# Optimization experiments

Hardware: AMD Instinct MI355X
Metric: run time of the kernel (lower is better)

## Reference

```python
import jax, jax.numpy as jnp
import numpy as np

N_NODES = 100000
N_EDGES = 1000000
D = 64
N_LAYERS = 3
LN_EPS = 1e-5


def setup_inputs() -> dict:
    key = jax.random.key(0)
    ks = jax.random.split(key, 12)
    s = 1.0 / np.sqrt(D)
    return {
        "feats": jax.random.normal(ks[0], (N_NODES, D), jnp.float32),
        "src": jax.random.randint(ks[1], (N_EDGES,), 0, N_NODES, jnp.int32),
        "dst": jax.random.randint(ks[2], (N_EDGES,), 0, N_NODES, jnp.int32),
        # GraphConv weights/biases (stacked over layers; in==hid==out==D)
        "conv_W": jax.random.normal(ks[3], (N_LAYERS, D, D), jnp.float32) * s,
        "conv_b": jnp.zeros((N_LAYERS, D), jnp.float32),
        # residual Linear per layer
        "res_W": jax.random.normal(ks[4], (N_LAYERS, D, D), jnp.float32) * s,
        "res_b": jnp.zeros((N_LAYERS, D), jnp.float32),
        # LayerNorm affine per layer
        "ln_g": jnp.ones((N_LAYERS, D), jnp.float32),
        "ln_b": jnp.zeros((N_LAYERS, D), jnp.float32),
        # final linear_prediction
        "pred_W": jax.random.normal(ks[5], (D, D), jnp.float32) * s,
        "pred_b": jnp.zeros((D,), jnp.float32),
    }


def _layer_norm(h, g, b):
    mu = jnp.mean(h, axis=-1, keepdims=True)
    var = jnp.mean(jnp.square(h - mu), axis=-1, keepdims=True)
    return (h - mu) * jax.lax.rsqrt(var + LN_EPS) * g + b


def reference(feats, src, dst, conv_W, conv_b, res_W, res_b, ln_g, ln_b, pred_W, pred_b):
    n = feats.shape[0]
    ones = jnp.ones(src.shape[0], feats.dtype)
    # DGL GraphConv norm='both', degrees clamped to >= 1
    out_deg = jnp.clip(jax.ops.segment_sum(ones, src, num_segments=n), 1.0, None)
    in_deg = jnp.clip(jax.ops.segment_sum(ones, dst, num_segments=n), 1.0, None)
    out_norm = jax.lax.rsqrt(out_deg)[:, None]  # [N,1]
    in_norm = jax.lax.rsqrt(in_deg)[:, None]

    h = feats
    h_final = jnp.zeros_like(feats)
    for i in range(N_LAYERS):
        # GraphConv: scale src, sum-aggregate over edges, scale dst, linear
        msg = (h * out_norm)[src]                                   # [E, D]
        agg = jax.ops.segment_sum(msg, dst, num_segments=n) * in_norm
        conv = agg @ conv_W[i] + conv_b[i]
        # residual linear + LayerNorm + relu (dropout p=0) + JK accumulate
        h = conv + h @ res_W[i] + res_b[i]
        h = jax.nn.relu(_layer_norm(h, ln_g[i], ln_b[i]))
        h_final = h_final + h
    return h_final @ pred_W + pred_b
```

## Files before the change

kernel.cpp:

```cpp
#include <hip/hip_runtime.h>
#include <hip/hip_bf16.h>

#define DD 64
#define NBLK 128
#define MAXBUK 1024
#define BSHIFT 7

typedef __attribute__((ext_vector_type(8))) short short8v;
typedef __attribute__((ext_vector_type(4))) float f32x4;

__device__ __forceinline__ unsigned pk_bf16(float a, float b) {
    __hip_bfloat162 h = __float22bfloat162_rn(make_float2(a, b));
    unsigned u; __builtin_memcpy(&u, &h, 4); return u;
}
__device__ __forceinline__ short f2bf_s(float f) {
    union { float f; unsigned u; } x; x.f = f;
    unsigned r = x.u + 0x7fff + ((x.u >> 16) & 1);
    return (short)(r >> 16);
}
__device__ __forceinline__ float bf_lo(unsigned u) { return __int_as_float(u << 16); }
__device__ __forceinline__ float bf_hi(unsigned u) { return __int_as_float(u & 0xffff0000u); }
__device__ __forceinline__ short8v u4_to_s8(uint4 u) {
    union { uint4 u; short8v s; } x; x.u = u; return x.s;
}
__device__ __forceinline__ int ofs_at(const int* __restrict__ c,
                                      const int* __restrict__ bs, int i) {
    return c[i] + bs[i >> 8];
}


__global__ __launch_bounds__(256) void part_count(
        const int* __restrict__ src, const int* __restrict__ dst,
        int* __restrict__ cnt, int E, int nbuk, int ce) {
    __shared__ int hd[MAXBUK], hs[MAXBUK];
    for (int i = threadIdx.x; i < MAXBUK; i += 256) { hd[i] = 0; hs[i] = 0; }
    __syncthreads();
    int e0 = blockIdx.x * ce;
    int e1 = min(e0 + ce, E);
    for (int e = e0 + (int)threadIdx.x; e < e1; e += 256) {
        atomicAdd(&hd[dst[e] >> BSHIFT], 1);
        atomicAdd(&hs[src[e] >> BSHIFT], 1);
    }
    __syncthreads();
    int L2 = nbuk * NBLK;
    for (int b = threadIdx.x; b < nbuk; b += 256) {
        cnt[b * NBLK + blockIdx.x]      = hd[b];
        cnt[L2 + b * NBLK + blockIdx.x] = hs[b];
    }
}

__global__ void scan1p(int* __restrict__ a, int* __restrict__ bsums, int L) {
    __shared__ int tmp[256];
    int gid = blockIdx.x * 256 + threadIdx.x;
    int v = (gid < L) ? a[gid] : 0;
    tmp[threadIdx.x] = v;
    __syncthreads();
    for (int off = 1; off < 256; off <<= 1) {
        int t = (threadIdx.x >= off) ? tmp[threadIdx.x - off] : 0;
        __syncthreads();
        tmp[threadIdx.x] += t;
        __syncthreads();
    }
    if (gid < L) a[gid] = tmp[threadIdx.x] - v;
    if (threadIdx.x == 255) bsums[blockIdx.x] = tmp[255];
}
__global__ void scan2p(int* __restrict__ bsums, int nb) {
    __shared__ int tmp[1024];
    int v = (threadIdx.x < (unsigned)nb) ? bsums[threadIdx.x] : 0;
    tmp[threadIdx.x] = v;
    __syncthreads();
    for (int off = 1; off < 1024; off <<= 1) {
        int t = (threadIdx.x >= off) ? tmp[threadIdx.x - off] : 0;
        __syncthreads();
        tmp[threadIdx.x] += t;
        __syncthreads();
    }
    if (threadIdx.x < (unsigned)nb) bsums[threadIdx.x] = tmp[threadIdx.x] - v;
}

__global__ __launch_bounds__(256) void part_scatter(
        const int* __restrict__ src, const int* __restrict__ dst,
        const int* __restrict__ cnt, const int* __restrict__ bsA,
        unsigned int* __restrict__ partD, unsigned char* __restrict__ partS,
        int E, int nbuk, int ce) {
    __shared__ int cd[MAXBUK], cs[MAXBUK];
    int L2 = nbuk * NBLK;
    for (int b = threadIdx.x; b < nbuk; b += 256) {
        cd[b] = ofs_at(cnt, bsA, b * NBLK + blockIdx.x);
        cs[b] = ofs_at(cnt, bsA, L2 + b * NBLK + blockIdx.x) - E;
    }
    __syncthreads();
    int e0 = blockIdx.x * ce;
    int e1 = min(e0 + ce, E);
    for (int e = e0 + (int)threadIdx.x; e < e1; e += 256) {
        int s = src[e], d = dst[e];
        int pd = atomicAdd(&cd[d >> BSHIFT], 1);
        partD[pd] = ((unsigned)(d & 127) << 17) | (unsigned)s;
        int ps = atomicAdd(&cs[s >> BSHIFT], 1);
        partS[ps] = (unsigned char)(s & 127);
    }
}

__global__ __launch_bounds__(256) void bucket_all(
        const unsigned int* __restrict__ partD, const unsigned char* __restrict__ partS,
        const int* __restrict__ cnt, const int* __restrict__ bsA,
        int* __restrict__ rowptr, int* __restrict__ esrc,
        float* __restrict__ inn, float* __restrict__ outn, float* __restrict__ rs,
        int E, int nbuk, int n) {
    __shared__ int hi[128], sc[128], cu[128], ho[128];
    int b = blockIdx.x, tid = threadIdx.x;
    int L2 = nbuk * NBLK;
    int e0 = ofs_at(cnt, bsA, b * NBLK);
    int e1 = (b + 1 < nbuk) ? ofs_at(cnt, bsA, (b + 1) * NBLK) : E;
    int f0 = ofs_at(cnt, bsA, L2 + b * NBLK) - E;
    int f1 = (b + 1 < nbuk) ? ofs_at(cnt, bsA, L2 + (b + 1) * NBLK) - E : E;
    if (tid < 128) { hi[tid] = 0; ho[tid] = 0; }
    __syncthreads();
    for (int e = e0 + tid; e < e1; e += 256) atomicAdd(&hi[partD[e] >> 17], 1);
    for (int e = f0 + tid; e < f1; e += 256) atomicAdd(&ho[(int)partS[e]], 1);
    __syncthreads();
    if (tid < 128) sc[tid] = hi[tid];
    __syncthreads();
    for (int off = 1; off < 128; off <<= 1) {
        int t = (tid < 128 && tid >= off) ? sc[tid - off] : 0;
        __syncthreads();
        if (tid < 128) sc[tid] += t;
        __syncthreads();
    }
    if (tid < 128) {
        int excl = e0 + sc[tid] - hi[tid];
        cu[tid] = excl;
        int v = (b << BSHIFT) + tid;
        if (v < n) {
            rowptr[v] = excl;
            inn[v] = rsqrtf((float)max(hi[tid], 1));
            float oc = (float)max(ho[tid], 1);
            outn[v] = rsqrtf(oc);
            rs[v]   = sqrtf(oc);
        }
    }
    if (b == 0 && tid == 0) rowptr[n] = E;
    __syncthreads();
    for (int e = e0 + tid; e < e1; e += 256) {
        unsigned u = partD[e];
        int p = atomicAdd(&cu[u >> 17], 1);
        esrc[p] = (int)(u & 0x1FFFFu);
    }
}

__global__ void scale_kernel(const float* __restrict__ feats, const float* __restrict__ outn,
                             unsigned short* __restrict__ hs, int n) {
    int idx = blockIdx.x * blockDim.x + threadIdx.x;
    if (idx < n * 8) {
        int v = idx >> 3;
        float s = outn[v];
        const float4* fp = (const float4*)feats + (size_t)idx * 2;
        float4 f0 = fp[0], f1 = fp[1];
        uint4 o;
        o.x = pk_bf16(f0.x * s, f0.y * s); o.y = pk_bf16(f0.z * s, f0.w * s);
        o.z = pk_bf16(f1.x * s, f1.y * s); o.w = pk_bf16(f1.z * s, f1.w * s);
        ((uint4*)hs)[idx] = o;
    }
}

__global__ __launch_bounds__(256) void gcn_kernel(
    const int* __restrict__ rowptr, const int* __restrict__ esrc,
    const float* __restrict__ inn, const float* __restrict__ rs,
    const float* __restrict__ outn,
    const unsigned short* __restrict__ hs_in,
    const float* __restrict__ Wc, const float* __restrict__ bc,
    const float* __restrict__ Wr, const float* __restrict__ br,
    const float* __restrict__ Wp, const float* __restrict__ pb,
    const float* __restrict__ g, const float* __restrict__ bb,
    unsigned short* __restrict__ hs_out, float* __restrict__ h_final,
    float* __restrict__ pred_out,
    int first, int last, int n)
{
    __shared__ __align__(16) short sWf[24 * 64 * 8];
    __shared__ __align__(16) short sXa[4][16 * 72];
    __shared__ float sEps[4 * 64];

    int lane = threadIdx.x & 63;
    int wave = threadIdx.x >> 6;
    int q   = lane & 15;
    int gg  = lane >> 4;
    int q8  = lane & 7;
    int o8  = lane >> 3;

    for (int idx = threadIdx.x; idx < 64; idx += blockDim.x) {
        sEps[idx]       = bc[idx] + br[idx];
        sEps[64 + idx]  = g[idx];
        sEps[128 + idx] = bb[idx];
        sEps[192 + idx] = pb[idx];
    }
    for (int f = wave * 6; f < wave * 6 + 6; ++f) {
        int mat = f >> 3, ft = (f >> 1) & 3, kc = f & 1;
        const float* Ws = (mat == 0) ? Wc : (mat == 1) ? Wr : Wp;
        int feat = ft * 16 + q;
        int k0 = kc * 32 + gg * 8;
        short8v fr;
        #pragma unroll
        for (int j = 0; j < 8; ++j) fr[j] = f2bf_s(Ws[(k0 + j) * DD + feat]);
        *(short8v*)&sWf[(f * 64 + lane) * 8] = fr;
    }
    __syncthreads();

    short* xrow_w = &sXa[wave][0];
    const short8v* wf = (const short8v*)sWf;
    int wgid = blockIdx.x * 4 + wave;
    int nwav = gridDim.x * 4;
    int ngrp = (n + 15) >> 4;

    for (int grp = wgid; grp < ngrp; grp += nwav) {
        int vbase = grp << 4;
        int vo = vbase + q;
        int vsel = min(vo, n - 1);

        const uint4* hrow = (const uint4*)(hs_in + (size_t)vsel * DD);
        uint4 bh0u = hrow[gg];
        uint4 bh1u = hrow[4 + gg];
        float rsv  = rs[vsel];
        float innv = inn[vsel];

        int rp = rowptr[min(vbase + min(lane, 16), n)];
        int stA = __shfl(rp, o8);     int dgA = __shfl(rp, o8 + 1) - stA;
        int stB = __shfl(rp, o8 + 8); int dgB = __shfl(rp, o8 + 9) - stB;

        #pragma unroll
        for (int hh = 0; hh < 2; ++hh) {
            int st = hh ? stB : stA;
            int dg = hh ? dgB : dgA;
            int mdg = dg;
            mdg = max(mdg, __shfl_xor(mdg, 8));
            mdg = max(mdg, __shfl_xor(mdg, 16));
            mdg = max(mdg, __shfl_xor(mdg, 32));

            float a[8];
            #pragma unroll
            for (int c = 0; c < 8; ++c) a[c] = 0.0f;

            int id0 = (0 < dg) ? esrc[st + 0] : 0;  float m0 = (0 < dg) ? 1.f : 0.f;
            int id1 = (1 < dg) ? esrc[st + 1] : 0;  float m1 = (1 < dg) ? 1.f : 0.f;
            int id2 = (2 < dg) ? esrc[st + 2] : 0;  float m2 = (2 < dg) ? 1.f : 0.f;
            int id3 = (3 < dg) ? esrc[st + 3] : 0;  float m3 = (3 < dg) ? 1.f : 0.f;

            for (int t = 0; t < mdg; t += 4) {
                uint4 r0 = *(const uint4*)(hs_in + (size_t)id0 * DD + q8 * 8);
                uint4 r1 = *(const uint4*)(hs_in + (size_t)id1 * DD + q8 * 8);
                uint4 r2 = *(const uint4*)(hs_in + (size_t)id2 * DD + q8 * 8);
                uint4 r3 = *(const uint4*)(hs_in + (size_t)id3 * DD + q8 * 8);
                float c0 = m0, c1 = m1, c2 = m2, c3 = m3;
                int t4 = t + 4;
                id0 = (t4 + 0 < dg) ? esrc[st + t4 + 0] : 0;  m0 = (t4 + 0 < dg) ? 1.f : 0.f;
                id1 = (t4 + 1 < dg) ? esrc[st + t4 + 1] : 0;  m1 = (t4 + 1 < dg) ? 1.f : 0.f;
                id2 = (t4 + 2 < dg) ? esrc[st + t4 + 2] : 0;  m2 = (t4 + 2 < dg) ? 1.f : 0.f;
                id3 = (t4 + 3 < dg) ? esrc[st + t4 + 3] : 0;  m3 = (t4 + 3 < dg) ? 1.f : 0.f;
                a[0] = fmaf(bf_lo(r0.x), c0, a[0]); a[1] = fmaf(bf_hi(r0.x), c0, a[1]);
                a[2] = fmaf(bf_lo(r0.y), c0, a[2]); a[3] = fmaf(bf_hi(r0.y), c0, a[3]);
                a[4] = fmaf(bf_lo(r0.z), c0, a[4]); a[5] = fmaf(bf_hi(r0.z), c0, a[5]);
                a[6] = fmaf(bf_lo(r0.w), c0, a[6]); a[7] = fmaf(bf_hi(r0.w), c0, a[7]);
                a[0] = fmaf(bf_lo(r1.x), c1, a[0]); a[1] = fmaf(bf_hi(r1.x), c1, a[1]);
                a[2] = fmaf(bf_lo(r1.y), c1, a[2]); a[3] = fmaf(bf_hi(r1.y), c1, a[3]);
                a[4] = fmaf(bf_lo(r1.z), c1, a[4]); a[5] = fmaf(bf_hi(r1.z), c1, a[5]);
                a[6] = fmaf(bf_lo(r1.w), c1, a[6]); a[7] = fmaf(bf_hi(r1.w), c1, a[7]);
                a[0] = fmaf(bf_lo(r2.x), c2, a[0]); a[1] = fmaf(bf_hi(r2.x), c2, a[1]);
                a[2] = fmaf(bf_lo(r2.y), c2, a[2]); a[3] = fmaf(bf_hi(r2.y), c2, a[3]);
                a[4] = fmaf(bf_lo(r2.z), c2, a[4]); a[5] = fmaf(bf_hi(r2.z), c2, a[5]);
                a[6] = fmaf(bf_lo(r2.w), c2, a[6]); a[7] = fmaf(bf_hi(r2.w), c2, a[7]);
                a[0] = fmaf(bf_lo(r3.x), c3, a[0]); a[1] = fmaf(bf_hi(r3.x), c3, a[1]);
                a[2] = fmaf(bf_lo(r3.y), c3, a[2]); a[3] = fmaf(bf_hi(r3.y), c3, a[3]);
                a[4] = fmaf(bf_lo(r3.z), c3, a[4]); a[5] = fmaf(bf_hi(r3.z), c3, a[5]);
                a[6] = fmaf(bf_lo(r3.w), c3, a[6]); a[7] = fmaf(bf_hi(r3.w), c3, a[7]);
            }

            uint4 w4;
            w4.x = pk_bf16(a[0], a[1]); w4.y = pk_bf16(a[2], a[3]);
            w4.z = pk_bf16(a[4], a[5]); w4.w = pk_bf16(a[6], a[7]);
            *(uint4*)&xrow_w[(hh * 8 + o8) * 72 + q8 * 8] = w4;
        }

        const short* xr = &xrow_w[q * 72];
        short8v ba0 = *(const short8v*)&xr[gg * 8];
        short8v ba1 = *(const short8v*)&xr[32 + gg * 8];
        short8v sh0 = u4_to_s8(bh0u);
        short8v sh1 = u4_to_s8(bh1u);

        f32x4 accC[4], accR[4];
        #pragma unroll
        for (int ft = 0; ft < 4; ++ft) {
            f32x4 c = {0.f, 0.f, 0.f, 0.f};
            c = __builtin_amdgcn_mfma_f32_16x16x32_bf16(wf[(ft * 2 + 0) * 64 + lane], ba0, c, 0, 0, 0);
            c = __builtin_amdgcn_mfma_f32_16x16x32_bf16(wf[(ft * 2 + 1) * 64 + lane], ba1, c, 0, 0, 0);
            accC[ft] = c;
            f32x4 r = {0.f, 0.f, 0.f, 0.f};
            r = __builtin_amdgcn_mfma_f32_16x16x32_bf16(wf[(8 + ft * 2 + 0) * 64 + lane], sh0, r, 0, 0, 0);
            r = __builtin_amdgcn_mfma_f32_16x16x32_bf16(wf[(8 + ft * 2 + 1) * 64 + lane], sh1, r, 0, 0, 0);
            accR[ft] = r;
        }

        f32x4 ac[4];
        #pragma unroll
        for (int ft = 0; ft < 4; ++ft) {
            float4 b4 = *(const float4*)&sEps[ft * 16 + gg * 4];
            ac[ft][0] = fmaf(innv, accC[ft][0], fmaf(rsv, accR[ft][0], b4.x));
            ac[ft][1] = fmaf(innv, accC[ft][1], fmaf(rsv, accR[ft][1], b4.y));
            ac[ft][2] = fmaf(innv, accC[ft][2], fmaf(rsv, accR[ft][2], b4.z));
            ac[ft][3] = fmaf(innv, accC[ft][3], fmaf(rsv, accR[ft][3], b4.w));
        }
        float s = 0.f;
        #pragma unroll
        for (int ft = 0; ft < 4; ++ft) s += ac[ft][0] + ac[ft][1] + ac[ft][2] + ac[ft][3];
        s += __shfl_xor(s, 16); s += __shfl_xor(s, 32);
        float mu = s * (1.0f / 64.0f);
        float vsum = 0.f;
        #pragma unroll
        for (int ft = 0; ft < 4; ++ft) {
            #pragma unroll
            for (int r = 0; r < 4; ++r) { float d = ac[ft][r] - mu; vsum += d * d; }
        }
        vsum += __shfl_xor(vsum, 16); vsum += __shfl_xor(vsum, 32);
        float rinv = rsqrtf(vsum * (1.0f / 64.0f) + 1e-5f);

        float4 yv[4];
        #pragma unroll
        for (int ft = 0; ft < 4; ++ft) {
            float4 g4 = *(const float4*)&sEps[64 + ft * 16 + gg * 4];
            float4 c4 = *(const float4*)&sEps[128 + ft * 16 + gg * 4];
            yv[ft].x = fmaxf((ac[ft][0] - mu) * rinv * g4.x + c4.x, 0.f);
            yv[ft].y = fmaxf((ac[ft][1] - mu) * rinv * g4.y + c4.y, 0.f);
            yv[ft].z = fmaxf((ac[ft][2] - mu) * rinv * g4.z + c4.z, 0.f);
            yv[ft].w = fmaxf((ac[ft][3] - mu) * rinv * g4.w + c4.w, 0.f);
        }

        if (!last) {
            if (vo < n) {
                float on = outn[vo];
                #pragma unroll
                for (int ft = 0; ft < 4; ++ft) {
                    size_t off = (size_t)vo * DD + ft * 16 + gg * 4;
                    uint2 p;
                    p.x = pk_bf16(yv[ft].x * on, yv[ft].y * on);
                    p.y = pk_bf16(yv[ft].z * on, yv[ft].w * on);
                    *(uint2*)&hs_out[off] = p;
                    if (first) {
                        *(float4*)&h_final[off] = yv[ft];
                    } else {
                        float4 hf = *(const float4*)&h_final[off];
                        hf.x += yv[ft].x; hf.y += yv[ft].y;
                        hf.z += yv[ft].z; hf.w += yv[ft].w;
                        *(float4*)&h_final[off] = hf;
                    }
                }
            }
        } else {
            #pragma unroll
            for (int ft = 0; ft < 4; ++ft) {
                float4 hf = make_float4(0.f, 0.f, 0.f, 0.f);
                if (vo < n) {
                    float4 old = *(const float4*)&h_final[(size_t)vo * DD + ft * 16 + gg * 4];
                    hf.x = old.x + yv[ft].x; hf.y = old.y + yv[ft].y;
                    hf.z = old.z + yv[ft].z; hf.w = old.w + yv[ft].w;
                }
                uint2 p;
                p.x = pk_bf16(hf.x, hf.y);
                p.y = pk_bf16(hf.z, hf.w);
                *(uint2*)&xrow_w[q * 72 + ft * 16 + gg * 4] = p;
            }
            short8v bp0 = *(const short8v*)&xr[gg * 8];
            short8v bp1 = *(const short8v*)&xr[32 + gg * 8];
            #pragma unroll
            for (int ft = 0; ft < 4; ++ft) {
                f32x4 p = {0.f, 0.f, 0.f, 0.f};
                p = __builtin_amdgcn_mfma_f32_16x16x32_bf16(wf[(16 + ft * 2 + 0) * 64 + lane], bp0, p, 0, 0, 0);
                p = __builtin_amdgcn_mfma_f32_16x16x32_bf16(wf[(16 + ft * 2 + 1) * 64 + lane], bp1, p, 0, 0, 0);
                if (vo < n) {
                    float4 b4 = *(const float4*)&sEps[192 + ft * 16 + gg * 4];
                    float4 o = make_float4(p[0] + b4.x, p[1] + b4.y, p[2] + b4.z, p[3] + b4.w);
                    *(float4*)&pred_out[(size_t)vo * DD + ft * 16 + gg * 4] = o;
                }
            }
        }
    }
}

extern "C" void kernel_launch(void* const* d_in, const int* in_sizes, int n_in,
                              void* d_out, int out_size, void* d_ws, size_t ws_size,
                              hipStream_t stream) {
    const float* feats  = (const float*)d_in[0];
    const int*   src    = (const int*)d_in[1];
    const int*   dst    = (const int*)d_in[2];
    const float* conv_W = (const float*)d_in[3];
    const float* conv_b = (const float*)d_in[4];
    const float* res_W  = (const float*)d_in[5];
    const float* res_b  = (const float*)d_in[6];
    const float* ln_g   = (const float*)d_in[7];
    const float* ln_b   = (const float*)d_in[8];
    const float* pred_W = (const float*)d_in[9];
    const float* pred_b = (const float*)d_in[10];

    int N = in_sizes[0] / DD;
    int E = in_sizes[1];

    int nbuk = (N + (1 << BSHIFT) - 1) >> BSHIFT;
    int ce   = (E + NBLK - 1) / NBLK;
    int L    = nbuk * NBLK * 2;
    int nb   = (L + 255) / 256;

    int*   rowptr = (int*)d_ws;
    int*   cnt    = rowptr + (N + 1);
    int*   bsA    = cnt + MAXBUK * NBLK * 2;
    int*   esrc   = bsA + 1024;
    float* outn   = (float*)(esrc + E);
    float* inn    = outn + N;
    float* rs     = inn + N;
    float* base   = (float*)(((uintptr_t)(rs + N) + 15) & ~(uintptr_t)15);
    unsigned short* hsA = (unsigned short*)base;
    unsigned short* hsB = (unsigned short*)(base + (size_t)N * 32);
    float* hfin  = base + (size_t)N * 64;
    unsigned int*  partD = (unsigned int*)hfin;
    unsigned char* partS = (unsigned char*)(partD + E);

    part_count  <<<NBLK, 256, 0, stream>>>(src, dst, cnt, E, nbuk, ce);
    scan1p      <<<nb, 256, 0, stream>>>(cnt, bsA, L);
    scan2p      <<<1, 1024, 0, stream>>>(bsA, nb);
    part_scatter<<<NBLK, 256, 0, stream>>>(src, dst, cnt, bsA, partD, partS, E, nbuk, ce);
    bucket_all  <<<nbuk, 256, 0, stream>>>(partD, partS, cnt, bsA, rowptr, esrc,
                                           inn, outn, rs, E, nbuk, N);
    scale_kernel<<<(N * 8 + 255) / 256, 256, 0, stream>>>(feats, outn, hsA, N);

    const unsigned short* ins[3]  = {hsA, hsB, hsA};
    unsigned short*       outs[3] = {hsB, hsA, hsB};
    for (int l = 0; l < 3; ++l) {
        gcn_kernel<<<1024, 256, 0, stream>>>(
            rowptr, esrc, inn, rs, outn, ins[l],
            conv_W + (size_t)l * DD * DD, conv_b + (size_t)l * DD,
            res_W  + (size_t)l * DD * DD, res_b  + (size_t)l * DD,
            pred_W, pred_b,
            ln_g   + (size_t)l * DD,      ln_b   + (size_t)l * DD,
            outs[l], hfin, (float*)d_out,
            (l == 0) ? 1 : 0, (l == 2) ? 1 : 0, N);
    }
}
```

Before: 297.1 us.

## Use atomic work-stealing for node groups and fuse feature scaling into bucket pass

Replaces the static grid-stride assignment of 16-node groups in the GCN layer kernel with a global atomic counter per layer, so waves pull work dynamically and balance the uneven in-degree load. The next group index is prefetched at the top of each iteration to hide the atomic latency. The separate scale/bf16 conversion kernel is folded into bucket_all, where each block scales its 128 nodes using out-norms held in shared memory, saving one launch. Counters are zeroed in part_count. This adds an atomic per group per wave and makes bucket_all longer.

```diff
diff --git a/kernel.cpp b/kernel.cpp
--- a/kernel.cpp
+++ b/kernel.cpp
@@ -31,8 +31,9 @@
 
 __global__ __launch_bounds__(256) void part_count(
         const int* __restrict__ src, const int* __restrict__ dst,
-        int* __restrict__ cnt, int E, int nbuk, int ce) {
+        int* __restrict__ cnt, int* __restrict__ wctr, int E, int nbuk, int ce) {
     __shared__ int hd[MAXBUK], hs[MAXBUK];
+    if (blockIdx.x == 0 && threadIdx.x < 3) wctr[threadIdx.x] = 0;
     for (int i = threadIdx.x; i < MAXBUK; i += 256) { hd[i] = 0; hs[i] = 0; }
     __syncthreads();
     int e0 = blockIdx.x * ce;
@@ -104,10 +105,13 @@
 __global__ __launch_bounds__(256) void bucket_all(
         const unsigned int* __restrict__ partD, const unsigned char* __restrict__ partS,
         const int* __restrict__ cnt, const int* __restrict__ bsA,
+        const float* __restrict__ feats,
         int* __restrict__ rowptr, int* __restrict__ esrc,
         float* __restrict__ inn, float* __restrict__ outn, float* __restrict__ rs,
+        unsigned short* __restrict__ hsv,
         int E, int nbuk, int n) {
     __shared__ int hi[128], sc[128], cu[128], ho[128];
+    __shared__ float son[128];
     int b = blockIdx.x, tid = threadIdx.x;
     int L2 = nbuk * NBLK;
     int e0 = ofs_at(cnt, bsA, b * NBLK);
@@ -127,15 +131,18 @@
         if (tid < 128) sc[tid] += t;
         __syncthreads();
     }
+    int nodeBase = b << BSHIFT;
     if (tid < 128) {
         int excl = e0 + sc[tid] - hi[tid];
         cu[tid] = excl;
-        int v = (b << BSHIFT) + tid;
+        float oc = (float)max(ho[tid], 1);
+        float on = rsqrtf(oc);
+        son[tid] = on;
+        int v = nodeBase + tid;
         if (v < n) {
             rowptr[v] = excl;
             inn[v] = rsqrtf((float)max(hi[tid], 1));
-            float oc = (float)max(ho[tid], 1);
-            outn[v] = rsqrtf(oc);
+            outn[v] = on;
             rs[v]   = sqrtf(oc);
         }
     }
@@ -146,20 +153,18 @@
         int p = atomicAdd(&cu[u >> 17], 1);
         esrc[p] = (int)(u & 0x1FFFFu);
     }
-}
-
-__global__ void scale_kernel(const float* __restrict__ feats, const float* __restrict__ outn,
-                             unsigned short* __restrict__ hs, int n) {
-    int idx = blockIdx.x * blockDim.x + threadIdx.x;
-    if (idx < n * 8) {
-        int v = idx >> 3;
-        float s = outn[v];
-        const float4* fp = (const float4*)feats + (size_t)idx * 2;
-        float4 f0 = fp[0], f1 = fp[1];
-        uint4 o;
-        o.x = pk_bf16(f0.x * s, f0.y * s); o.y = pk_bf16(f0.z * s, f0.w * s);
-        o.z = pk_bf16(f1.x * s, f1.y * s); o.w = pk_bf16(f1.z * s, f1.w * s);
-        ((uint4*)hs)[idx] = o;
+    for (int idx = tid; idx < 128 * 8; idx += 256) {
+        int vl = idx >> 3, c = idx & 7;
+        int v = nodeBase + vl;
+        if (v < n) {
+            float s = son[vl];
+            const float4* fp = (const float4*)(feats + (size_t)v * DD) + c * 2;
+            float4 g0 = fp[0], g1 = fp[1];
+            uint4 o;
+            o.x = pk_bf16(g0.x * s, g0.y * s); o.y = pk_bf16(g0.z * s, g0.w * s);
+            o.z = pk_bf16(g1.x * s, g1.y * s); o.w = pk_bf16(g1.z * s, g1.w * s);
+            *(uint4*)&hsv[(size_t)v * DD + c * 8] = o;
+        }
     }
 }
 
@@ -173,7 +178,7 @@
     const float* __restrict__ Wp, const float* __restrict__ pb,
     const float* __restrict__ g, const float* __restrict__ bb,
     unsigned short* __restrict__ hs_out, float* __restrict__ h_final,
-    float* __restrict__ pred_out,
+    float* __restrict__ pred_out, int* __restrict__ wctr,
     int first, int last, int n)
 {
     __shared__ __align__(16) short sWf[24 * 64 * 8];
@@ -207,11 +212,16 @@
 
     short* xrow_w = &sXa[wave][0];
     const short8v* wf = (const short8v*)sWf;
-    int wgid = blockIdx.x * 4 + wave;
-    int nwav = gridDim.x * 4;
     int ngrp = (n + 15) >> 4;
 
-    for (int grp = wgid; grp < ngrp; grp += nwav) {
+    int grp = 0;
+    if (lane == 0) grp = atomicAdd(wctr, 1);
+    grp = __shfl(grp, 0);
+
+    while (grp < ngrp) {
+        int gnext = 0;
+        if (lane == 0) gnext = atomicAdd(wctr, 1);
+
         int vbase = grp << 4;
         int vo = vbase + q;
         int vsel = min(vo, n - 1);
@@ -380,6 +390,8 @@
                 }
             }
         }
+
+        grp = __shfl(gnext, 0);
     }
 }
 
@@ -409,7 +421,8 @@
     int*   rowptr = (int*)d_ws;
     int*   cnt    = rowptr + (N + 1);
     int*   bsA    = cnt + MAXBUK * NBLK * 2;
-    int*   esrc   = bsA + 1024;
+    int*   wctr   = bsA + 1024;
+    int*   esrc   = wctr + 256;
     float* outn   = (float*)(esrc + E);
     float* inn    = outn + N;
     float* rs     = inn + N;
@@ -420,13 +433,12 @@
     unsigned int*  partD = (unsigned int*)hfin;
     unsigned char* partS = (unsigned char*)(partD + E);
 
-    part_count  <<<NBLK, 256, 0, stream>>>(src, dst, cnt, E, nbuk, ce);
+    part_count  <<<NBLK, 256, 0, stream>>>(src, dst, cnt, wctr, E, nbuk, ce);
     scan1p      <<<nb, 256, 0, stream>>>(cnt, bsA, L);
     scan2p      <<<1, 1024, 0, stream>>>(bsA, nb);
     part_scatter<<<NBLK, 256, 0, stream>>>(src, dst, cnt, bsA, partD, partS, E, nbuk, ce);
-    bucket_all  <<<nbuk, 256, 0, stream>>>(partD, partS, cnt, bsA, rowptr, esrc,
-                                           inn, outn, rs, E, nbuk, N);
-    scale_kernel<<<(N * 8 + 255) / 256, 256, 0, stream>>>(feats, outn, hsA, N);
+    bucket_all  <<<nbuk, 256, 0, stream>>>(partD, partS, cnt, bsA, feats, rowptr, esrc,
+                                           inn, outn, rs, hsA, E, nbuk, N);
 
     const unsigned short* ins[3]  = {hsA, hsB, hsA};
     unsigned short*       outs[3] = {hsB, hsA, hsB};
@@ -437,7 +449,7 @@
             res_W  + (size_t)l * DD * DD, res_b  + (size_t)l * DD,
             pred_W, pred_b,
             ln_g   + (size_t)l * DD,      ln_b   + (size_t)l * DD,
-            outs[l], hfin, (float*)d_out,
+            outs[l], hfin, (float*)d_out, wctr + l,
             (l == 0) ? 1 : 0, (l == 2) ? 1 : 0, N);
     }
 }
```

Result: slower. 554.5 us (+86.6%).
